# Performance work log

Hardware: AMD Instinct MI355X
Metric: run time of the kernel (lower is better)

Reference implementation:

```python
import jax, jax.numpy as jnp
import numpy as np

N = 50000

def gcn_conv(x, src, dst, W, b, num_nodes):
    # x: [N, Fin], src/dst: [E'] (self-loops already included)
    h = x @ W  # [N, Fout]
    ones = jnp.ones(src.shape[0], dtype=h.dtype)
    deg = jax.ops.segment_sum(ones, dst, num_segments=num_nodes)  # in-degree incl. self-loop
    dinv = jnp.where(deg > 0, jax.lax.rsqrt(deg), 0.0)
    norm = dinv[src] * dinv[dst]  # [E']
    msg = h[src] * norm[:, None]  # gather + scale
    out = jax.ops.segment_sum(msg, dst, num_segments=num_nodes)  # scatter-add
    return out + b

def setup_inputs() -> dict:
    key = jax.random.key(0)
    k1, k2, k3, k4, k5, k6 = jax.random.split(key, 6)
    E = 800000
    Fin, H, Fout = 128, 64, 32
    x = jax.random.normal(k1, (N, Fin), dtype=jnp.float32)
    edge_index = jax.random.randint(k2, (2, E), 0, N, dtype=jnp.int32)
    edge_attr = jax.random.normal(k3, (E, 8), dtype=jnp.float32)
    s1 = 1.0 / np.sqrt(Fin)
    s2 = 1.0 / np.sqrt(H)
    W1 = jax.random.uniform(k4, (Fin, H), dtype=jnp.float32, minval=-s1, maxval=s1)
    b1 = jnp.zeros((H,), dtype=jnp.float32)
    W2 = jax.random.uniform(k5, (H, Fout), dtype=jnp.float32, minval=-s2, maxval=s2)
    b2 = jnp.zeros((Fout,), dtype=jnp.float32)
    return {"x": x, "edge_index": edge_index, "edge_attr": edge_attr,
            "W1": W1, "b1": b1, "W2": W2, "b2": b2}

def reference(x, edge_index, edge_attr, W1, b1, W2, b2):
    num_nodes = x.shape[0]
    loop = jnp.arange(num_nodes, dtype=edge_index.dtype)
    src = jnp.concatenate([edge_index[0], loop])
    dst = jnp.concatenate([edge_index[1], loop])
    h = gcn_conv(x, src, dst, W1, b1, num_nodes)
    h = jax.nn.relu(h)
    # dropout is identity in eval mode
    out = gcn_conv(h, src, dst, W2, b2, num_nodes)
    return out
```

## Files before the change

### kernel.cpp

```cpp
#include <hip/hip_runtime.h>
#include <hip/hip_fp16.h>
#include <cstdint>
#include <cstddef>


#define SHIFT 8
#define NPB 256
#define CHUNK 8192
#define IMG_CAP 6144

__global__ __launch_bounds__(256) void hist_kernel(const int* __restrict__ dst, int E, int nWG,
                                                   int B, int* __restrict__ hist) {
  __shared__ int h[256];
  int t = threadIdx.x, w = blockIdx.x;
  for (int i = t; i < B; i += 256) h[i] = 0;
  __syncthreads();
  int beg = w * CHUNK, end = min(beg + CHUNK, E);
  for (int i = beg + t; i < end; i += 256) atomicAdd(&h[dst[i] >> SHIFT], 1);
  __syncthreads();
  for (int i = t; i < B; i += 256) hist[i * nWG + w] = h[i];
}

__global__ __launch_bounds__(256) void rowscan_kernel(const int* __restrict__ hist, int nWG,
                                                      int* __restrict__ rowscan, int* __restrict__ total) {
  int b = blockIdx.x, t = threadIdx.x;
  int v = (t < nWG) ? hist[b * nWG + t] : 0;
  int lane = t & 63, wid = t >> 6;
  int x = v;
#pragma unroll
  for (int o = 1; o < 64; o <<= 1) { int y = __shfl_up(x, o, 64); if (lane >= o) x += y; }
  __shared__ int wsum[4];
  if (lane == 63) wsum[wid] = x;
  __syncthreads();
  int bw = 0;
  for (int i = 0; i < wid; ++i) bw += wsum[i];
  int incl = bw + x;
  if (t < nWG) rowscan[b * nWG + t] = incl - v;
  if (t == nWG - 1) total[b] = incl;
}

__global__ __launch_bounds__(256) void scatterkeys_kernel(const int* __restrict__ src,
                                                          const int* __restrict__ dst, int E, int nWG,
                                                          int B, const int* __restrict__ hist,
                                                          const int* __restrict__ rowscan,
                                                          const int* __restrict__ total,
                                                          unsigned* __restrict__ keys) {
  __shared__ int loffs[256], cur[256], gb[256];
  __shared__ int wsum[4];
  __shared__ unsigned image[CHUNK];
  __shared__ int gdst[CHUNK];
  int t = threadIdx.x, w = blockIdx.x;
  int lane = t & 63, wid = t >> 6;
  {
    int v = (t < B) ? total[t] : 0;
    int x = v;
#pragma unroll
    for (int o = 1; o < 64; o <<= 1) { int y = __shfl_up(x, o, 64); if (lane >= o) x += y; }
    if (lane == 63) wsum[wid] = x;
    __syncthreads();
    int bw = 0;
    for (int i = 0; i < wid; ++i) bw += wsum[i];
    int excl = bw + x - v;
    if (t < B) gb[t] = excl + rowscan[t * nWG + w];
  }
  __syncthreads();
  {
    int v = (t < B) ? hist[t * nWG + w] : 0;
    int x = v;
#pragma unroll
    for (int o = 1; o < 64; o <<= 1) { int y = __shfl_up(x, o, 64); if (lane >= o) x += y; }
    if (lane == 63) wsum[wid] = x;
    __syncthreads();
    int bw = 0;
    for (int i = 0; i < wid; ++i) bw += wsum[i];
    int excl = bw + x - v;
    if (t < B) { loffs[t] = excl; cur[t] = excl; }
  }
  __syncthreads();
  int beg = w * CHUNK, end = min(beg + CHUNK, E);
  for (int i = beg + t; i < end; i += 256) {
    int d = dst[i], s = src[i];
    int b = d >> SHIFT;
    int p = atomicAdd(&cur[b], 1);
    image[p] = ((unsigned)(d & (NPB - 1)) << 16) | (unsigned)s;
    gdst[p] = gb[b] + (p - loffs[b]);
  }
  __syncthreads();
  int n = end - beg;
  for (int i = t; i < n; i += 256) keys[gdst[i]] = image[i];
}

__global__ __launch_bounds__(256) void bucket_build_kernel(const unsigned* __restrict__ keys,
                                                           const int* __restrict__ total, int B, int N,
                                                           int* __restrict__ csr, int* __restrict__ eoff,
                                                           int* __restrict__ ecnt, float* __restrict__ dinv) {
  __shared__ int cnt[NPB], loffs[NPB], cur[NPB];
  __shared__ int red[4];
  __shared__ int image[IMG_CAP];
  int b = blockIdx.x, t = threadIdx.x;
  int lane = t & 63, wid = t >> 6;
  int part = 0;
  for (int i = t; i < b; i += 256) part += total[i];
#pragma unroll
  for (int o = 32; o > 0; o >>= 1) part += __shfl_down(part, o, 64);
  if (lane == 0) red[wid] = part;
  __syncthreads();
  int gbeg = red[0] + red[1] + red[2] + red[3];
  int m = total[b];
  int gend = gbeg + m;
  int nb = b << SHIFT;
  int nn = min(NPB, N - nb);
  cnt[t] = 0;
  __syncthreads();
  for (int i = gbeg + t; i < gend; i += 256) atomicAdd(&cnt[keys[i] >> 16], 1);
  __syncthreads();
  if (t < 64) {
    int v0 = cnt[4 * t], v1 = cnt[4 * t + 1], v2 = cnt[4 * t + 2], v3 = cnt[4 * t + 3];
    int s = v0 + v1 + v2 + v3, x = s;
#pragma unroll
    for (int o = 1; o < 64; o <<= 1) { int y = __shfl_up(x, o, 64); if (t >= o) x += y; }
    int e = x - s;
    loffs[4 * t] = e;                 cur[4 * t] = e;
    loffs[4 * t + 1] = e + v0;        cur[4 * t + 1] = e + v0;
    loffs[4 * t + 2] = e + v0 + v1;   cur[4 * t + 2] = e + v0 + v1;
    loffs[4 * t + 3] = e + v0 + v1 + v2; cur[4 * t + 3] = e + v0 + v1 + v2;
  }
  __syncthreads();
  for (int n2 = t; n2 < nn; n2 += 256) {
    eoff[nb + n2] = gbeg + loffs[n2];
    ecnt[nb + n2] = cnt[n2];
    dinv[nb + n2] = 1.0f / sqrtf((float)(cnt[n2] + 1));
  }
  if (m <= IMG_CAP) {
    for (int i = gbeg + t; i < gend; i += 256) {
      unsigned k = keys[i];
      int p = atomicAdd(&cur[k >> 16], 1);
      image[p] = (int)(k & 0xFFFFu);
    }
    __syncthreads();
    for (int i = t; i < m; i += 256) csr[gbeg + i] = image[i];
  } else {
    for (int i = gbeg + t; i < gend; i += 256) {
      unsigned k = keys[i];
      int p = atomicAdd(&cur[k >> 16], 1);
      csr[gbeg + p] = (int)(k & 0xFFFFu);
    }
  }
}

__global__ __launch_bounds__(256) void gemm1_kernel(
    const float* __restrict__ x, const float* __restrict__ W1,
    const float* __restrict__ dinv, __half* __restrict__ h1s, int N) {
  __shared__ float ws[128 * 64];
  __shared__ float xs[64 * 128];
  const int t = threadIdx.x;
  const int rowBase = blockIdx.x * 64;
  float4* ws4 = (float4*)ws;
  float4* xs4 = (float4*)xs;
  for (int i = t; i < 128 * 16; i += 256) ws4[i] = ((const float4*)W1)[i];
  for (int i = t; i < 64 * 32; i += 256) {
    int r = i >> 5, kq = i & 31;
    int row = rowBase + r;
    float4 v = make_float4(0.f, 0.f, 0.f, 0.f);
    if (row < N) v = ((const float4*)x)[(size_t)row * 32 + kq];
    xs4[r * 32 + (kq ^ ((r >> 2) & 7))] = v;
  }
  __syncthreads();
  const int g = t & 15;
  const int rg = t >> 4;
  const int swz = rg & 7;
  float acc[4][4] = {};
  for (int kq = 0; kq < 32; ++kq) {
    float4 a[4];
#pragma unroll
    for (int j = 0; j < 4; ++j) a[j] = xs4[(4 * rg + j) * 32 + (kq ^ swz)];
    float4 w[4];
#pragma unroll
    for (int kk = 0; kk < 4; ++kk) w[kk] = ws4[(4 * kq + kk) * 16 + g];
#pragma unroll
    for (int j = 0; j < 4; ++j) {
      acc[j][0] += a[j].x * w[0].x + a[j].y * w[1].x + a[j].z * w[2].x + a[j].w * w[3].x;
      acc[j][1] += a[j].x * w[0].y + a[j].y * w[1].y + a[j].z * w[2].y + a[j].w * w[3].y;
      acc[j][2] += a[j].x * w[0].z + a[j].y * w[1].z + a[j].z * w[2].z + a[j].w * w[3].z;
      acc[j][3] += a[j].x * w[0].w + a[j].y * w[1].w + a[j].z * w[2].w + a[j].w * w[3].w;
    }
  }
#pragma unroll
  for (int j = 0; j < 4; ++j) {
    int row = rowBase + 4 * rg + j;
    if (row < N) {
      float dv = dinv[row];
      union { __half2 h2[2]; float2 f2v; } u;
      u.h2[0] = __floats2half2_rn(acc[j][0] * dv, acc[j][1] * dv);
      u.h2[1] = __floats2half2_rn(acc[j][2] * dv, acc[j][3] * dv);
      ((float2*)h1s)[(size_t)row * 16 + g] = u.f2v;
    }
  }
}

__global__ __launch_bounds__(256) void gather64_gemm2_kernel(
    const __half* __restrict__ h1s, const int* __restrict__ csr, const int* __restrict__ eoff,
    const int* __restrict__ ecnt, const float* __restrict__ dinv, const float* __restrict__ b1,
    const float* __restrict__ W2, __half* __restrict__ h2s, int N) {
  __shared__ float w2s[64 * 32];
  __shared__ float arow[8 * 64];
  int t = threadIdx.x;
  float4* w2s4 = (float4*)w2s;
  for (int i = t; i < 512; i += 256) w2s4[i] = ((const float4*)W2)[i];
  __syncthreads();
  int slot = t >> 5;
  int d = blockIdx.x * 8 + slot;
  if (d >= N) return;
  int f2 = t & 31;
  const __half2* h1p = (const __half2*)h1s;
  int beg = eoff[d], m = ecnt[d];
  float2 a0 = __half22float2(h1p[(size_t)d * 32 + f2]);
  float2 aA = make_float2(0.f, 0.f), aB = make_float2(0.f, 0.f), aC = make_float2(0.f, 0.f);
  int j = 0;
  for (; j + 16 <= m; j += 16) {
    int s[16];
#pragma unroll
    for (int i = 0; i < 16; ++i) s[i] = csr[beg + j + i];
    __half2 v[16];
#pragma unroll
    for (int i = 0; i < 16; ++i) v[i] = h1p[(size_t)s[i] * 32 + f2];
#pragma unroll
    for (int i = 0; i < 16; ++i) {
      float2 f = __half22float2(v[i]);
      float2* ac = (i & 3) == 0 ? &a0 : (i & 3) == 1 ? &aA : (i & 3) == 2 ? &aB : &aC;
      ac->x += f.x; ac->y += f.y;
    }
  }
  for (; j + 4 <= m; j += 4) {
    int s0 = csr[beg + j], s1 = csr[beg + j + 1], s2 = csr[beg + j + 2], s3 = csr[beg + j + 3];
    __half2 v0 = h1p[(size_t)s0 * 32 + f2], v1 = h1p[(size_t)s1 * 32 + f2];
    __half2 v2 = h1p[(size_t)s2 * 32 + f2], v3 = h1p[(size_t)s3 * 32 + f2];
    float2 f0 = __half22float2(v0), f1 = __half22float2(v1);
    float2 f2v = __half22float2(v2), f3 = __half22float2(v3);
    a0.x += f0.x; a0.y += f0.y; aA.x += f1.x; aA.y += f1.y;
    aB.x += f2v.x; aB.y += f2v.y; aC.x += f3.x; aC.y += f3.y;
  }
  for (; j < m; ++j) {
    float2 f = __half22float2(h1p[(size_t)csr[beg + j] * 32 + f2]);
    a0.x += f.x; a0.y += f.y;
  }
  float sx = (a0.x + aA.x) + (aB.x + aC.x);
  float sy = (a0.y + aA.y) + (aB.y + aC.y);
  float dv = dinv[d];
  float2 bb = ((const float2*)b1)[f2];
  float ax = fmaxf(sx * dv + bb.x, 0.f);
  float ay = fmaxf(sy * dv + bb.y, 0.f);
  ((float2*)arow)[slot * 32 + f2] = make_float2(ax, ay);
  const float* ar = &arow[slot * 64];
  float s = 0.f;
#pragma unroll
  for (int kk = 0; kk < 64; ++kk) s += ar[kk] * w2s[kk * 32 + f2];
  h2s[(size_t)d * 32 + f2] = __float2half_rn(s * dv);
}

__global__ __launch_bounds__(256) void gather32_kernel(
    const __half* __restrict__ h2s, const int* __restrict__ csr, const int* __restrict__ eoff,
    const int* __restrict__ ecnt, const float* __restrict__ dinv, const float* __restrict__ b2,
    float* __restrict__ out, int N) {
  int t = threadIdx.x;
  int d = blockIdx.x * 16 + (t >> 4);
  if (d >= N) return;
  int f2 = t & 15;
  const __half2* h2p = (const __half2*)h2s;
  int beg = eoff[d], m = ecnt[d];
  float2 a0 = __half22float2(h2p[(size_t)d * 16 + f2]);
  float2 aA = make_float2(0.f, 0.f), aB = make_float2(0.f, 0.f), aC = make_float2(0.f, 0.f);
  int j = 0;
  for (; j + 16 <= m; j += 16) {
    int s[16];
#pragma unroll
    for (int i = 0; i < 16; ++i) s[i] = csr[beg + j + i];
    __half2 v[16];
#pragma unroll
    for (int i = 0; i < 16; ++i) v[i] = h2p[(size_t)s[i] * 16 + f2];
#pragma unroll
    for (int i = 0; i < 16; ++i) {
      float2 f = __half22float2(v[i]);
      float2* ac = (i & 3) == 0 ? &a0 : (i & 3) == 1 ? &aA : (i & 3) == 2 ? &aB : &aC;
      ac->x += f.x; ac->y += f.y;
    }
  }
  for (; j + 4 <= m; j += 4) {
    int s0 = csr[beg + j], s1 = csr[beg + j + 1], s2 = csr[beg + j + 2], s3 = csr[beg + j + 3];
    __half2 v0 = h2p[(size_t)s0 * 16 + f2], v1 = h2p[(size_t)s1 * 16 + f2];
    __half2 v2 = h2p[(size_t)s2 * 16 + f2], v3 = h2p[(size_t)s3 * 16 + f2];
    float2 f0 = __half22float2(v0), f1 = __half22float2(v1);
    float2 f2v = __half22float2(v2), f3 = __half22float2(v3);
    a0.x += f0.x; a0.y += f0.y; aA.x += f1.x; aA.y += f1.y;
    aB.x += f2v.x; aB.y += f2v.y; aC.x += f3.x; aC.y += f3.y;
  }
  for (; j < m; ++j) {
    float2 f = __half22float2(h2p[(size_t)csr[beg + j] * 16 + f2]);
    a0.x += f.x; a0.y += f.y;
  }
  float sx = (a0.x + aA.x) + (aB.x + aC.x);
  float sy = (a0.y + aA.y) + (aB.y + aC.y);
  float dv = dinv[d];
  float2 bb = ((const float2*)b2)[f2];
  ((float2*)out)[(size_t)d * 16 + f2] = make_float2(sx * dv + bb.x, sy * dv + bb.y);
}

extern "C" void kernel_launch(void* const* d_in, const int* in_sizes, int n_in,
                              void* d_out, int out_size, void* d_ws, size_t ws_size,
                              hipStream_t stream) {
  const float* x = (const float*)d_in[0];
  const int* edge_index = (const int*)d_in[1];
  const float* W1 = (const float*)d_in[3];
  const float* b1 = (const float*)d_in[4];
  const float* W2 = (const float*)d_in[5];
  const float* b2 = (const float*)d_in[6];
  float* out = (float*)d_out;

  const int N = in_sizes[0] / 128;
  const int E = in_sizes[1] / 2;
  const int* src = edge_index;
  const int* dst = edge_index + E;

  const int B = (N + NPB - 1) >> SHIFT;
  const int nWG = (E + CHUNK - 1) / CHUNK;

  char* ws = (char*)d_ws;
  size_t off = 0;
  auto alloc = [&](size_t bytes) -> void* {
    void* p = ws + off;
    off += (bytes + 255) & ~(size_t)255;
    return p;
  };
  unsigned* keys = (unsigned*)alloc((size_t)E * 4);
  int* csr = (int*)alloc((size_t)E * 4);
  int* hist = (int*)alloc((size_t)B * nWG * 4);
  int* rowscan = (int*)alloc((size_t)B * nWG * 4);
  int* total = (int*)alloc((size_t)B * 4);
  int* eoff = (int*)alloc((size_t)N * 4);
  int* ecnt = (int*)alloc((size_t)N * 4);
  float* dinv = (float*)alloc((size_t)N * 4);
  __half* h1s = (__half*)alloc((size_t)N * 64 * 2);
  __half* h2s = (__half*)alloc((size_t)N * 32 * 2);

  hist_kernel<<<nWG, 256, 0, stream>>>(dst, E, nWG, B, hist);
  rowscan_kernel<<<B, 256, 0, stream>>>(hist, nWG, rowscan, total);
  scatterkeys_kernel<<<nWG, 256, 0, stream>>>(src, dst, E, nWG, B, hist, rowscan, total, keys);
  bucket_build_kernel<<<B, 256, 0, stream>>>(keys, total, B, N, csr, eoff, ecnt, dinv);
  gemm1_kernel<<<(N + 63) / 64, 256, 0, stream>>>(x, W1, dinv, h1s, N);
  gather64_gemm2_kernel<<<(N + 7) / 8, 256, 0, stream>>>(h1s, csr, eoff, ecnt, dinv, b1, W2, h2s, N);
  gather32_kernel<<<(N + 15) / 16, 256, 0, stream>>>(h2s, csr, eoff, ecnt, dinv, b2, out, N);
}
```

Before: 107.2 us.

## Split gather-GEMM2 into separate kernels and shrink scatter chunk shared memory

The fused gather64+GEMM2 kernel is split in two. The gather now writes the ReLU activations as fp16 to a new buffer, and a separate register-tiled GEMM kernel with a swizzled shared-memory layout computes h2s. The scatter-keys kernel stops keeping a gdst array and instead packs the bucket id into the top byte of each key to recompute destinations. CHUNK is halved, which cuts shared memory and raises occupancy. In exchange there is an extra global round trip for the activations and one more kernel launch.

```diff
diff --git a/kernel.cpp b/kernel.cpp
--- a/kernel.cpp
+++ b/kernel.cpp
@@ -6,7 +6,7 @@
 
 #define SHIFT 8
 #define NPB 256
-#define CHUNK 8192
+#define CHUNK 4096
 #define IMG_CAP 6144
 
 __global__ __launch_bounds__(256) void hist_kernel(const int* __restrict__ dst, int E, int nWG,
@@ -48,7 +48,6 @@
   __shared__ int loffs[256], cur[256], gb[256];
   __shared__ int wsum[4];
   __shared__ unsigned image[CHUNK];
-  __shared__ int gdst[CHUNK];
   int t = threadIdx.x, w = blockIdx.x;
   int lane = t & 63, wid = t >> 6;
   {
@@ -82,12 +81,15 @@
     int d = dst[i], s = src[i];
     int b = d >> SHIFT;
     int p = atomicAdd(&cur[b], 1);
-    image[p] = ((unsigned)(d & (NPB - 1)) << 16) | (unsigned)s;
-    gdst[p] = gb[b] + (p - loffs[b]);
+    image[p] = ((unsigned)b << 24) | ((unsigned)(d & (NPB - 1)) << 16) | (unsigned)s;
   }
   __syncthreads();
   int n = end - beg;
-  for (int i = t; i < n; i += 256) keys[gdst[i]] = image[i];
+  for (int i = t; i < n; i += 256) {
+    unsigned k = image[i];
+    int b = (int)(k >> 24);
+    keys[gb[b] + (i - loffs[b])] = k;
+  }
 }
 
 __global__ __launch_bounds__(256) void bucket_build_kernel(const unsigned* __restrict__ keys,
@@ -112,7 +114,7 @@
   int nn = min(NPB, N - nb);
   cnt[t] = 0;
   __syncthreads();
-  for (int i = gbeg + t; i < gend; i += 256) atomicAdd(&cnt[keys[i] >> 16], 1);
+  for (int i = gbeg + t; i < gend; i += 256) atomicAdd(&cnt[(keys[i] >> 16) & 0xFF], 1);
   __syncthreads();
   if (t < 64) {
     int v0 = cnt[4 * t], v1 = cnt[4 * t + 1], v2 = cnt[4 * t + 2], v3 = cnt[4 * t + 3];
@@ -134,7 +136,7 @@
   if (m <= IMG_CAP) {
     for (int i = gbeg + t; i < gend; i += 256) {
       unsigned k = keys[i];
-      int p = atomicAdd(&cur[k >> 16], 1);
+      int p = atomicAdd(&cur[(k >> 16) & 0xFF], 1);
       image[p] = (int)(k & 0xFFFFu);
     }
     __syncthreads();
@@ -142,7 +144,7 @@
   } else {
     for (int i = gbeg + t; i < gend; i += 256) {
       unsigned k = keys[i];
-      int p = atomicAdd(&cur[k >> 16], 1);
+      int p = atomicAdd(&cur[(k >> 16) & 0xFF], 1);
       csr[gbeg + p] = (int)(k & 0xFFFFu);
     }
   }
@@ -198,16 +200,11 @@
   }
 }
 
-__global__ __launch_bounds__(256) void gather64_gemm2_kernel(
+__global__ __launch_bounds__(256) void gather64_kernel(
     const __half* __restrict__ h1s, const int* __restrict__ csr, const int* __restrict__ eoff,
     const int* __restrict__ ecnt, const float* __restrict__ dinv, const float* __restrict__ b1,
-    const float* __restrict__ W2, __half* __restrict__ h2s, int N) {
-  __shared__ float w2s[64 * 32];
-  __shared__ float arow[8 * 64];
+    __half* __restrict__ a1, int N) {
   int t = threadIdx.x;
-  float4* w2s4 = (float4*)w2s;
-  for (int i = t; i < 512; i += 256) w2s4[i] = ((const float4*)W2)[i];
-  __syncthreads();
   int slot = t >> 5;
   int d = blockIdx.x * 8 + slot;
   if (d >= N) return;
@@ -250,12 +247,62 @@
   float2 bb = ((const float2*)b1)[f2];
   float ax = fmaxf(sx * dv + bb.x, 0.f);
   float ay = fmaxf(sy * dv + bb.y, 0.f);
-  ((float2*)arow)[slot * 32 + f2] = make_float2(ax, ay);
-  const float* ar = &arow[slot * 64];
-  float s = 0.f;
-#pragma unroll
-  for (int kk = 0; kk < 64; ++kk) s += ar[kk] * w2s[kk * 32 + f2];
-  h2s[(size_t)d * 32 + f2] = __float2half_rn(s * dv);
+  ((__half2*)a1)[(size_t)d * 32 + f2] = __floats2half2_rn(ax, ay);
+}
+
+__global__ __launch_bounds__(256) void gemm2h_kernel(
+    const __half* __restrict__ a1, const float* __restrict__ W2,
+    const float* __restrict__ dinv, __half* __restrict__ h2s, int N) {
+  __shared__ float ws[64 * 32];
+  __shared__ float xs[128 * 64];
+  const int t = threadIdx.x;
+  const int rowBase = blockIdx.x * 128;
+  float4* ws4 = (float4*)ws;
+  float4* xs4 = (float4*)xs;
+  for (int i = t; i < 64 * 8; i += 256) ws4[i] = ((const float4*)W2)[i];
+  for (int i = t; i < 128 * 16; i += 256) {
+    int r = i >> 4, kq = i & 15;
+    int row = rowBase + r;
+    float4 v = make_float4(0.f, 0.f, 0.f, 0.f);
+    if (row < N) {
+      union { float2 f2v; __half2 h2[2]; } u;
+      u.f2v = ((const float2*)a1)[(size_t)row * 16 + kq];
+      float2 lo = __half22float2(u.h2[0]), hi = __half22float2(u.h2[1]);
+      v = make_float4(lo.x, lo.y, hi.x, hi.y);
+    }
+    xs4[r * 16 + (kq ^ ((r >> 2) & 7))] = v;
+  }
+  __syncthreads();
+  const int g = t & 7;
+  const int rg = t >> 3;
+  const int swz = rg & 7;
+  float acc[4][4] = {};
+  for (int kq = 0; kq < 16; ++kq) {
+    float4 a[4];
+#pragma unroll
+    for (int j = 0; j < 4; ++j) a[j] = xs4[(4 * rg + j) * 16 + (kq ^ swz)];
+    float4 w[4];
+#pragma unroll
+    for (int kk = 0; kk < 4; ++kk) w[kk] = ws4[(4 * kq + kk) * 8 + g];
+#pragma unroll
+    for (int j = 0; j < 4; ++j) {
+      acc[j][0] += a[j].x * w[0].x + a[j].y * w[1].x + a[j].z * w[2].x + a[j].w * w[3].x;
+      acc[j][1] += a[j].x * w[0].y + a[j].y * w[1].y + a[j].z * w[2].y + a[j].w * w[3].y;
+      acc[j][2] += a[j].x * w[0].z + a[j].y * w[1].z + a[j].z * w[2].z + a[j].w * w[3].z;
+      acc[j][3] += a[j].x * w[0].w + a[j].y * w[1].w + a[j].z * w[2].w + a[j].w * w[3].w;
+    }
+  }
+#pragma unroll
+  for (int j = 0; j < 4; ++j) {
+    int row = rowBase + 4 * rg + j;
+    if (row < N) {
+      float dv = dinv[row];
+      union { __half2 h2[2]; float2 f2v; } u;
+      u.h2[0] = __floats2half2_rn(acc[j][0] * dv, acc[j][1] * dv);
+      u.h2[1] = __floats2half2_rn(acc[j][2] * dv, acc[j][3] * dv);
+      ((float2*)h2s)[(size_t)row * 8 + g] = u.f2v;
+    }
+  }
 }
 
 __global__ __launch_bounds__(256) void gather32_kernel(
@@ -340,6 +387,7 @@
   int* ecnt = (int*)alloc((size_t)N * 4);
   float* dinv = (float*)alloc((size_t)N * 4);
   __half* h1s = (__half*)alloc((size_t)N * 64 * 2);
+  __half* a1 = (__half*)alloc((size_t)N * 64 * 2);
   __half* h2s = (__half*)alloc((size_t)N * 32 * 2);
 
   hist_kernel<<<nWG, 256, 0, stream>>>(dst, E, nWG, B, hist);
@@ -347,6 +395,7 @@
   scatterkeys_kernel<<<nWG, 256, 0, stream>>>(src, dst, E, nWG, B, hist, rowscan, total, keys);
   bucket_build_kernel<<<B, 256, 0, stream>>>(keys, total, B, N, csr, eoff, ecnt, dinv);
   gemm1_kernel<<<(N + 63) / 64, 256, 0, stream>>>(x, W1, dinv, h1s, N);
-  gather64_gemm2_kernel<<<(N + 7) / 8, 256, 0, stream>>>(h1s, csr, eoff, ecnt, dinv, b1, W2, h2s, N);
+  gather64_kernel<<<(N + 7) / 8, 256, 0, stream>>>(h1s, csr, eoff, ecnt, dinv, b1, a1, N);
+  gemm2h_kernel<<<(N + 127) / 128, 256, 0, stream>>>(a1, W2, dinv, h2s, N);
   gather32_kernel<<<(N + 15) / 16, 256, 0, stream>>>(h2s, csr, eoff, ecnt, dinv, b2, out, N);
 }
```

New measurement: 112.0 us. +4.5%, slower.

## Pack bucket into sort keys, shrink CSR indices to 16-bit, halve chunk size

Applied to the files above, without the earlier changes.

The scatter-keys kernel now stores the destination bucket in the top 8 bits of each key and recomputes the global slot from it. This removes the per-chunk shared gdst array and cuts shared-memory use, and the chunk size is halved so more workgroups run. The CSR source-index array becomes unsigned short, halving the index bytes read by both gather kernels. It still relies on N < 65536 and on fewer than 256 buckets, which the earlier 16-bit key packing already assumed.

```diff
diff --git a/kernel.cpp b/kernel.cpp
--- a/kernel.cpp
+++ b/kernel.cpp
@@ -6,7 +6,7 @@
 
 #define SHIFT 8
 #define NPB 256
-#define CHUNK 8192
+#define CHUNK 4096
 #define IMG_CAP 6144
 
 __global__ __launch_bounds__(256) void hist_kernel(const int* __restrict__ dst, int E, int nWG,
@@ -48,7 +48,6 @@
   __shared__ int loffs[256], cur[256], gb[256];
   __shared__ int wsum[4];
   __shared__ unsigned image[CHUNK];
-  __shared__ int gdst[CHUNK];
   int t = threadIdx.x, w = blockIdx.x;
   int lane = t & 63, wid = t >> 6;
   {
@@ -82,18 +81,23 @@
     int d = dst[i], s = src[i];
     int b = d >> SHIFT;
     int p = atomicAdd(&cur[b], 1);
-    image[p] = ((unsigned)(d & (NPB - 1)) << 16) | (unsigned)s;
-    gdst[p] = gb[b] + (p - loffs[b]);
+    image[p] = ((unsigned)b << 24) | ((unsigned)(d & (NPB - 1)) << 16) | (unsigned)s;
   }
   __syncthreads();
   int n = end - beg;
-  for (int i = t; i < n; i += 256) keys[gdst[i]] = image[i];
+  for (int i = t; i < n; i += 256) {
+    unsigned k = image[i];
+    int b = (int)(k >> 24);
+    keys[gb[b] + (i - loffs[b])] = k;
+  }
 }
 
 __global__ __launch_bounds__(256) void bucket_build_kernel(const unsigned* __restrict__ keys,
                                                            const int* __restrict__ total, int B, int N,
-                                                           int* __restrict__ csr, int* __restrict__ eoff,
-                                                           int* __restrict__ ecnt, float* __restrict__ dinv) {
+                                                           unsigned short* __restrict__ csr,
+                                                           int* __restrict__ eoff,
+                                                           int* __restrict__ ecnt,
+                                                           float* __restrict__ dinv) {
   __shared__ int cnt[NPB], loffs[NPB], cur[NPB];
   __shared__ int red[4];
   __shared__ int image[IMG_CAP];
@@ -112,7 +116,7 @@
   int nn = min(NPB, N - nb);
   cnt[t] = 0;
   __syncthreads();
-  for (int i = gbeg + t; i < gend; i += 256) atomicAdd(&cnt[keys[i] >> 16], 1);
+  for (int i = gbeg + t; i < gend; i += 256) atomicAdd(&cnt[(keys[i] >> 16) & 0xFF], 1);
   __syncthreads();
   if (t < 64) {
     int v0 = cnt[4 * t], v1 = cnt[4 * t + 1], v2 = cnt[4 * t + 2], v3 = cnt[4 * t + 3];
@@ -134,16 +138,16 @@
   if (m <= IMG_CAP) {
     for (int i = gbeg + t; i < gend; i += 256) {
       unsigned k = keys[i];
-      int p = atomicAdd(&cur[k >> 16], 1);
+      int p = atomicAdd(&cur[(k >> 16) & 0xFF], 1);
       image[p] = (int)(k & 0xFFFFu);
     }
     __syncthreads();
-    for (int i = t; i < m; i += 256) csr[gbeg + i] = image[i];
+    for (int i = t; i < m; i += 256) csr[gbeg + i] = (unsigned short)image[i];
   } else {
     for (int i = gbeg + t; i < gend; i += 256) {
       unsigned k = keys[i];
-      int p = atomicAdd(&cur[k >> 16], 1);
-      csr[gbeg + p] = (int)(k & 0xFFFFu);
+      int p = atomicAdd(&cur[(k >> 16) & 0xFF], 1);
+      csr[gbeg + p] = (unsigned short)(k & 0xFFFFu);
     }
   }
 }
@@ -199,8 +203,9 @@
 }
 
 __global__ __launch_bounds__(256) void gather64_gemm2_kernel(
-    const __half* __restrict__ h1s, const int* __restrict__ csr, const int* __restrict__ eoff,
-    const int* __restrict__ ecnt, const float* __restrict__ dinv, const float* __restrict__ b1,
+    const __half* __restrict__ h1s, const unsigned short* __restrict__ csr,
+    const int* __restrict__ eoff, const int* __restrict__ ecnt,
+    const float* __restrict__ dinv, const float* __restrict__ b1,
     const float* __restrict__ W2, __half* __restrict__ h2s, int N) {
   __shared__ float w2s[64 * 32];
   __shared__ float arow[8 * 64];
@@ -218,15 +223,15 @@
   float2 aA = make_float2(0.f, 0.f), aB = make_float2(0.f, 0.f), aC = make_float2(0.f, 0.f);
   int j = 0;
   for (; j + 16 <= m; j += 16) {
-    int s[16];
-#pragma unroll
-    for (int i = 0; i < 16; ++i) s[i] = csr[beg + j + i];
-    __half2 v[16];
-#pragma unroll
-    for (int i = 0; i < 16; ++i) v[i] = h1p[(size_t)s[i] * 32 + f2];
+    int s_[16];
+#pragma unroll
+    for (int i = 0; i < 16; ++i) s_[i] = csr[beg + j + i];
+    __half2 v_[16];
+#pragma unroll
+    for (int i = 0; i < 16; ++i) v_[i] = h1p[(size_t)s_[i] * 32 + f2];
 #pragma unroll
     for (int i = 0; i < 16; ++i) {
-      float2 f = __half22float2(v[i]);
+      float2 f = __half22float2(v_[i]);
       float2* ac = (i & 3) == 0 ? &a0 : (i & 3) == 1 ? &aA : (i & 3) == 2 ? &aB : &aC;
       ac->x += f.x; ac->y += f.y;
     }
@@ -259,8 +264,9 @@
 }
 
 __global__ __launch_bounds__(256) void gather32_kernel(
-    const __half* __restrict__ h2s, const int* __restrict__ csr, const int* __restrict__ eoff,
-    const int* __restrict__ ecnt, const float* __restrict__ dinv, const float* __restrict__ b2,
+    const __half* __restrict__ h2s, const unsigned short* __restrict__ csr,
+    const int* __restrict__ eoff, const int* __restrict__ ecnt,
+    const float* __restrict__ dinv, const float* __restrict__ b2,
     float* __restrict__ out, int N) {
   int t = threadIdx.x;
   int d = blockIdx.x * 16 + (t >> 4);
@@ -272,15 +278,15 @@
   float2 aA = make_float2(0.f, 0.f), aB = make_float2(0.f, 0.f), aC = make_float2(0.f, 0.f);
   int j = 0;
   for (; j + 16 <= m; j += 16) {
-    int s[16];
-#pragma unroll
-    for (int i = 0; i < 16; ++i) s[i] = csr[beg + j + i];
-    __half2 v[16];
-#pragma unroll
-    for (int i = 0; i < 16; ++i) v[i] = h2p[(size_t)s[i] * 16 + f2];
+    int s_[16];
+#pragma unroll
+    for (int i = 0; i < 16; ++i) s_[i] = csr[beg + j + i];
+    __half2 v_[16];
+#pragma unroll
+    for (int i = 0; i < 16; ++i) v_[i] = h2p[(size_t)s_[i] * 16 + f2];
 #pragma unroll
     for (int i = 0; i < 16; ++i) {
-      float2 f = __half22float2(v[i]);
+      float2 f = __half22float2(v_[i]);
       float2* ac = (i & 3) == 0 ? &a0 : (i & 3) == 1 ? &aA : (i & 3) == 2 ? &aB : &aC;
       ac->x += f.x; ac->y += f.y;
     }
@@ -332,7 +338,7 @@
     return p;
   };
   unsigned* keys = (unsigned*)alloc((size_t)E * 4);
-  int* csr = (int*)alloc((size_t)E * 4);
+  unsigned short* csr = (unsigned short*)alloc((size_t)E * 2);
   int* hist = (int*)alloc((size_t)B * nWG * 4);
   int* rowscan = (int*)alloc((size_t)B * nWG * 4);
   int* total = (int*)alloc((size_t)B * 4);
```

Result: faster. 98.61 us (-8.0%).
